# Performance work log

Hardware: AMD Instinct MI355X
Metric: run time of the kernel (lower is better)

The kernel has to match this reference:

```python
import jax, jax.numpy as jnp
import numpy as np

D_IN = 1024
D_OUT = 1024
NUM_HEADS = 16
HEAD_DIM = D_OUT // NUM_HEADS


def setup_inputs() -> dict:
    key = jax.random.key(0)
    ks = jax.random.split(key, 6)
    scale = 0.02
    x = jax.random.normal(ks[0], (2, 2048, D_IN), dtype=jnp.float32)
    Wq = jax.random.normal(ks[1], (D_IN, D_OUT), dtype=jnp.float32) * scale
    Wk = jax.random.normal(ks[2], (D_IN, D_OUT), dtype=jnp.float32) * scale
    Wv = jax.random.normal(ks[3], (D_IN, D_OUT), dtype=jnp.float32) * scale
    Wo = jax.random.normal(ks[4], (D_OUT, D_OUT), dtype=jnp.float32) * scale
    bo = jax.random.normal(ks[5], (D_OUT,), dtype=jnp.float32) * scale
    return {"x": x, "Wq": Wq, "Wk": Wk, "Wv": Wv, "Wo": Wo, "bo": bo}


def reference(x, Wq, Wk, Wv, Wo, bo):
    b, T, _ = x.shape
    h, dh = NUM_HEADS, HEAD_DIM
    # QKV projections (no bias), split heads: [b,T,d_out] -> [b,h,T,dh]
    q = (x @ Wq).reshape(b, T, h, dh).transpose(0, 2, 1, 3)
    k = (x @ Wk).reshape(b, T, h, dh).transpose(0, 2, 1, 3)
    v = (x @ Wv).reshape(b, T, h, dh).transpose(0, 2, 1, 3)
    # scaled dot-product scores with causal mask
    scores = jnp.einsum("bhqd,bhkd->bhqk", q, k) / jnp.sqrt(jnp.float32(dh))
    causal = jnp.tril(jnp.ones((T, T), dtype=bool))  # True = allowed
    scores = jnp.where(causal, scores, -jnp.inf)
    attn = jax.nn.softmax(scores, axis=-1)
    # dropout p=0.0 -> identity
    ctx = jnp.einsum("bhqk,bhkd->bhqd", attn, v)
    ctx = ctx.transpose(0, 2, 1, 3).reshape(b, T, h * dh)
    return ctx @ Wo + bo
```

## Files before the change

kernel.cpp:

```cpp
#include <hip/hip_runtime.h>

typedef __attribute__((ext_vector_type(8))) __bf16 bf16x8;
typedef __attribute__((ext_vector_type(4))) __bf16 bf16x4;
typedef __attribute__((ext_vector_type(4))) float  f32x4;

static constexpr int TSEQ    = 2048;
static constexpr int DMODEL  = 1024;
static constexpr int HD      = 64;
static constexpr int VSTRIDE = 2080;

#define AS1 __attribute__((address_space(1)))
#define AS3 __attribute__((address_space(3)))
#define SW(r) ((((r) & 12) >> 1) | ((r) & 1))

__global__ __launch_bounds__(256) void k_prep(const float* __restrict__ x,
    const float* __restrict__ w0, const float* __restrict__ w1,
    const float* __restrict__ w2, const float* __restrict__ w3,
    __bf16* __restrict__ xbf, __bf16* __restrict__ wt_all) {
  __shared__ float tile[32][33];
  const int blk = blockIdx.x;
  const int tid = threadIdx.x;
  if (blk < 4096) {
    size_t i = ((size_t)blk * 256 + tid) * 4;
    float4 v = *(const float4*)(x + i);
    bf16x4 o = { (__bf16)v.x, (__bf16)v.y, (__bf16)v.z, (__bf16)v.w };
    *(bf16x4*)(xbf + i) = o;
    return;
  }
  const int tz = blk - 4096;
  const int wi = tz >> 10;
  const int tl = tz & 1023;
  const int n0 = (tl & 31) * 32, k0 = (tl >> 5) * 32;
  const float* w = wi == 0 ? w0 : wi == 1 ? w1 : wi == 2 ? w2 : w3;
  __bf16* out = wt_all + (size_t)wi * DMODEL * DMODEL;
  const int tx = tid & 31, ty0 = (tid >> 5) * 4;
#pragma unroll
  for (int j = 0; j < 4; j++)
    tile[ty0 + j][tx] = w[(size_t)(k0 + ty0 + j) * DMODEL + n0 + tx];
  __syncthreads();
#pragma unroll
  for (int j = 0; j < 4; j++)
    out[(size_t)(n0 + ty0 + j) * DMODEL + k0 + tx] = (__bf16)tile[tx][ty0 + j];
}

__device__ __forceinline__ void gemm_mainloop(const __bf16* __restrict__ A,
                                              const __bf16* __restrict__ Bt,
                                              int bm, int bn,
                                              __bf16* At, __bf16* Bl,
                                              f32x4 acc[4][4]) {
  const int tid  = threadIdx.x;
  const int lane = tid & 63;
  const int l15  = lane & 15, quad = lane >> 4;
  const int wv   = tid >> 6;
  const int wm   = (wv >> 1) * 64, wn = (wv & 1) * 64;
  const int s0   = wv * 2;
  const int srow = lane >> 2;
  const int scol = (lane & 3) << 3;
  for (int k0 = 0; k0 < 1024; k0 += 32) {
    __syncthreads();
#pragma unroll
    for (int ss = 0; ss < 2; ss++) {
      const int s   = s0 + ss;
      const int row = s * 16 + srow;
      const __bf16* ga = A  + (size_t)(bm + row) * 1024 + k0 + scol;
      const __bf16* gb = Bt + (size_t)(bn + row) * 1024 + k0 + scol;
      __builtin_amdgcn_global_load_lds((const AS1 void*)ga,
                                       (AS3 void*)(At + s * 512), 16, 0, 0);
      __builtin_amdgcn_global_load_lds((const AS1 void*)gb,
                                       (AS3 void*)(Bl + s * 512), 16, 0, 0);
    }
    __syncthreads();
    bf16x8 af[4], bfr[4];
#pragma unroll
    for (int mt = 0; mt < 4; mt++)
      af[mt] = *(const bf16x8*)(At + (wm + mt * 16 + l15) * 32 + quad * 8);
#pragma unroll
    for (int nt = 0; nt < 4; nt++)
      bfr[nt] = *(const bf16x8*)(Bl + (wn + nt * 16 + l15) * 32 + quad * 8);
#pragma unroll
    for (int mt = 0; mt < 4; mt++)
#pragma unroll
      for (int nt = 0; nt < 4; nt++)
        acc[mt][nt] = __builtin_amdgcn_mfma_f32_16x16x32_bf16(
            af[mt], bfr[nt], acc[mt][nt], 0, 0, 0);
  }
}

__global__ __launch_bounds__(256) void k_gemm_qkv(const __bf16* __restrict__ xbf,
    const __bf16* __restrict__ wt_all, __bf16* __restrict__ qws,
    __bf16* __restrict__ kws, __bf16* __restrict__ vtws) {
  __shared__ __bf16 At[128 * 32];
  __shared__ __bf16 Bl[128 * 32];
  const int which = blockIdx.z;
  const __bf16* wt = wt_all + (size_t)which * DMODEL * DMODEL;
  const int bm = blockIdx.y * 128, bn = blockIdx.x * 128;
  f32x4 acc[4][4];
  const f32x4 z = {0.f, 0.f, 0.f, 0.f};
#pragma unroll
  for (int mt = 0; mt < 4; mt++)
#pragma unroll
    for (int nt = 0; nt < 4; nt++) acc[mt][nt] = z;
  gemm_mainloop(xbf, wt, bm, bn, At, Bl, acc);
  const int lane = threadIdx.x & 63;
  const int l15 = lane & 15, quad = lane >> 4;
  const int wv = threadIdx.x >> 6;
  const int wm = (wv >> 1) * 64, wn = (wv & 1) * 64;
#pragma unroll
  for (int mt = 0; mt < 4; mt++)
#pragma unroll
    for (int nt = 0; nt < 4; nt++)
#pragma unroll
      for (int r = 0; r < 4; r++) {
        int m = bm + wm + mt * 16 + quad * 4 + r;
        int n = bn + wn + nt * 16 + l15;
        int b = m >> 11, t = m & 2047;
        int h = n >> 6,  d = n & 63;
        int bh = b * 16 + h;
        float av = acc[mt][nt][r];
        if (which == 0)      qws[((size_t)bh * TSEQ + t) * HD + d] = (__bf16)(av * 0.18033688f);
        else if (which == 1) kws[((size_t)bh * TSEQ + t) * HD + d] = (__bf16)av;
        else                 vtws[((size_t)bh * HD + d) * VSTRIDE + t] = (__bf16)av;
      }
}

__global__ __launch_bounds__(256) void k_attn(const __bf16* __restrict__ qws,
    const __bf16* __restrict__ kws, const __bf16* __restrict__ vtws,
    __bf16* __restrict__ ctx) {
  const int bh = blockIdx.x & 31;
  const int a  = 15 - (blockIdx.x >> 5);
  const int tcnt = 2 * a + 2;
  const int tid = threadIdx.x;
  const int lane = tid & 63, wv = tid >> 6;
  const int l15 = lane & 15, quad = lane >> 4;
  const __bf16* qp = qws  + (size_t)bh * TSEQ * HD;
  const __bf16* kp = kws  + (size_t)bh * TSEQ * HD;
  const __bf16* vp = vtws + (size_t)bh * HD * VSTRIDE;
  const int b = bh >> 4, h = bh & 15;
  const int qbase = a * 128 + wv * 32;

  __shared__ __align__(16) __bf16 kbuf[2][64 * 64];
  __shared__ __align__(16) __bf16 vbuf[2][64 * 64];
  __shared__ __align__(16) __bf16 plds[4][32 * 64];

  const int sr = tid >> 3;
  const int c8 = tid & 7;

  bf16x8 aq[2][2];
#pragma unroll
  for (int mt = 0; mt < 2; mt++)
#pragma unroll
    for (int kb = 0; kb < 2; kb++)
      aq[mt][kb] = *(const bf16x8*)(qp + (size_t)(qbase + mt * 16 + l15) * HD + kb * 32 + quad * 8);

  bf16x8 kreg[2], vreg[2];
  kreg[0] = *(const bf16x8*)(kp + (size_t)sr * HD + c8 * 8);
  kreg[1] = *(const bf16x8*)(kp + (size_t)(sr + 32) * HD + c8 * 8);
  vreg[0] = *(const bf16x8*)(vp + (size_t)sr * VSTRIDE + c8 * 8);
  vreg[1] = *(const bf16x8*)(vp + (size_t)(sr + 32) * VSTRIDE + c8 * 8);
  *(bf16x8*)(kbuf[0] + sr * 64 + ((c8 ^ SW(sr)) << 3))             = kreg[0];
  *(bf16x8*)(kbuf[0] + (sr + 32) * 64 + ((c8 ^ SW(sr + 32)) << 3)) = kreg[1];
  *(bf16x8*)(vbuf[0] + sr * 64 + ((c8 ^ SW(sr)) << 3))             = vreg[0];
  *(bf16x8*)(vbuf[0] + (sr + 32) * 64 + ((c8 ^ SW(sr + 32)) << 3)) = vreg[1];
  __syncthreads();

  float lpart[2][4] = {{0.f, 0.f, 0.f, 0.f}, {0.f, 0.f, 0.f, 0.f}};
  const f32x4 z = {0.f, 0.f, 0.f, 0.f};
  f32x4 acc[2][4];
#pragma unroll
  for (int mt = 0; mt < 2; mt++)
#pragma unroll
    for (int dt = 0; dt < 4; dt++) acc[mt][dt] = z;

  for (int t = 0; t < tcnt; t++) {
    const int cur = t & 1;
    if (t + 1 < tcnt) {
      const int ktn = (t + 1) * 64;
      kreg[0] = *(const bf16x8*)(kp + (size_t)(ktn + sr) * HD + c8 * 8);
      kreg[1] = *(const bf16x8*)(kp + (size_t)(ktn + sr + 32) * HD + c8 * 8);
      vreg[0] = *(const bf16x8*)(vp + (size_t)sr * VSTRIDE + ktn + c8 * 8);
      vreg[1] = *(const bf16x8*)(vp + (size_t)(sr + 32) * VSTRIDE + ktn + c8 * 8);
    }

    const bool skipall = (t * 64) > (qbase + 31);
    if (!skipall) {
      const bool full = (t * 64 + 63) <= qbase;
      f32x4 sarr[2][4];
#pragma unroll
      for (int mt = 0; mt < 2; mt++)
#pragma unroll
        for (int nt = 0; nt < 4; nt++) sarr[mt][nt] = z;
#pragma unroll
      for (int kb = 0; kb < 2; kb++)
#pragma unroll
        for (int nt = 0; nt < 4; nt++) {
          const int row = nt * 16 + l15;
          bf16x8 bk = *(const bf16x8*)(kbuf[cur] + row * 64 + (((kb * 4 + quad) ^ SW(row)) << 3));
#pragma unroll
          for (int mt = 0; mt < 2; mt++)
            sarr[mt][nt] = __builtin_amdgcn_mfma_f32_16x16x32_bf16(aq[mt][kb], bk, sarr[mt][nt], 0, 0, 0);
        }
      if (full) {
#pragma unroll
        for (int mt = 0; mt < 2; mt++)
#pragma unroll
          for (int r = 0; r < 4; r++) {
            const int prow = mt * 16 + quad * 4 + r;
#pragma unroll
            for (int nt = 0; nt < 4; nt++) {
              float p = __builtin_amdgcn_exp2f(sarr[mt][nt][r]);
              lpart[mt][r] += p;
              plds[wv][prow * 64 + ((nt * 16 + l15) ^ (SW(prow) << 3))] = (__bf16)p;
            }
          }
      } else {
#pragma unroll
        for (int mt = 0; mt < 2; mt++)
#pragma unroll
          for (int r = 0; r < 4; r++) {
            const int prow = mt * 16 + quad * 4 + r;
            const int qglob = qbase + prow;
#pragma unroll
            for (int nt = 0; nt < 4; nt++) {
              const int kglob = t * 64 + nt * 16 + l15;
              float p = (kglob <= qglob) ? __builtin_amdgcn_exp2f(sarr[mt][nt][r]) : 0.f;
              lpart[mt][r] += p;
              plds[wv][prow * 64 + ((nt * 16 + l15) ^ (SW(prow) << 3))] = (__bf16)p;
            }
          }
      }
#pragma unroll
      for (int kb = 0; kb < 2; kb++) {
        bf16x8 pa[2];
#pragma unroll
        for (int mt = 0; mt < 2; mt++) {
          const int row = mt * 16 + l15;
          pa[mt] = *(const bf16x8*)(&plds[wv][row * 64 + (((kb * 4 + quad) ^ SW(row)) << 3)]);
        }
#pragma unroll
        for (int dt = 0; dt < 4; dt++) {
          const int rowv = dt * 16 + l15;
          bf16x8 bv = *(const bf16x8*)(vbuf[cur] + rowv * 64 + (((kb * 4 + quad) ^ SW(rowv)) << 3));
#pragma unroll
          for (int mt = 0; mt < 2; mt++)
            acc[mt][dt] = __builtin_amdgcn_mfma_f32_16x16x32_bf16(pa[mt], bv, acc[mt][dt], 0, 0, 0);
        }
      }
    }

    if (t + 1 < tcnt) {
      const int nxt = cur ^ 1;
      *(bf16x8*)(kbuf[nxt] + sr * 64 + ((c8 ^ SW(sr)) << 3))             = kreg[0];
      *(bf16x8*)(kbuf[nxt] + (sr + 32) * 64 + ((c8 ^ SW(sr + 32)) << 3)) = kreg[1];
      *(bf16x8*)(vbuf[nxt] + sr * 64 + ((c8 ^ SW(sr)) << 3))             = vreg[0];
      *(bf16x8*)(vbuf[nxt] + (sr + 32) * 64 + ((c8 ^ SW(sr + 32)) << 3)) = vreg[1];
    }
    __syncthreads();
  }

#pragma unroll
  for (int mt = 0; mt < 2; mt++)
#pragma unroll
    for (int r = 0; r < 4; r++) {
      float l = lpart[mt][r];
      l += __shfl_xor(l, 1, 64);
      l += __shfl_xor(l, 2, 64);
      l += __shfl_xor(l, 4, 64);
      l += __shfl_xor(l, 8, 64);
      const float linv = 1.f / l;
      const int qrow = qbase + mt * 16 + quad * 4 + r;
#pragma unroll
      for (int dt = 0; dt < 4; dt++)
        ctx[((size_t)(b * TSEQ + qrow)) * DMODEL + h * 64 + dt * 16 + l15] =
            (__bf16)(acc[mt][dt][r] * linv);
    }
}

__global__ __launch_bounds__(256) void k_gemm_out(const __bf16* __restrict__ ctx,
    const __bf16* __restrict__ wot, const float* __restrict__ bo,
    float* __restrict__ out) {
  __shared__ __bf16 At[128 * 32];
  __shared__ __bf16 Bl[128 * 32];
  const int bm = blockIdx.y * 128, bn = blockIdx.x * 128;
  f32x4 acc[4][4];
  const f32x4 z = {0.f, 0.f, 0.f, 0.f};
#pragma unroll
  for (int mt = 0; mt < 4; mt++)
#pragma unroll
    for (int nt = 0; nt < 4; nt++) acc[mt][nt] = z;
  gemm_mainloop(ctx, wot, bm, bn, At, Bl, acc);
  const int lane = threadIdx.x & 63;
  const int l15 = lane & 15, quad = lane >> 4;
  const int wv = threadIdx.x >> 6;
  const int wm = (wv >> 1) * 64, wn = (wv & 1) * 64;
#pragma unroll
  for (int mt = 0; mt < 4; mt++)
#pragma unroll
    for (int nt = 0; nt < 4; nt++)
#pragma unroll
      for (int r = 0; r < 4; r++) {
        int m = bm + wm + mt * 16 + quad * 4 + r;
        int n = bn + wn + nt * 16 + l15;
        out[(size_t)m * DMODEL + n] = acc[mt][nt][r] + bo[n];
      }
}

extern "C" void kernel_launch(void* const* d_in, const int* in_sizes, int n_in,
                              void* d_out, int out_size, void* d_ws, size_t ws_size,
                              hipStream_t stream) {
  const float* x  = (const float*)d_in[0];
  const float* Wq = (const float*)d_in[1];
  const float* Wk = (const float*)d_in[2];
  const float* Wv = (const float*)d_in[3];
  const float* Wo = (const float*)d_in[4];
  const float* bo = (const float*)d_in[5];
  float* out = (float*)d_out;

  __bf16* xbf  = (__bf16*)d_ws;
  __bf16* wt   = xbf  + (size_t)4096 * 1024;
  __bf16* qws  = wt   + (size_t)4 * 1024 * 1024;
  __bf16* kws  = qws  + (size_t)32 * 2048 * 64;
  __bf16* vtws = kws  + (size_t)32 * 2048 * 64;
  __bf16* ctx  = xbf;

  k_prep<<<8192, 256, 0, stream>>>(x, Wq, Wk, Wv, Wo, xbf, wt);
  k_gemm_qkv<<<dim3(8, 32, 3), 256, 0, stream>>>(xbf, wt, qws, kws, vtws);
  k_attn<<<512, 256, 0, stream>>>(qws, kws, vtws, ctx);
  k_gemm_out<<<dim3(8, 32), 256, 0, stream>>>(ctx, wt + (size_t)3 * 1024 * 1024, bo, out);
}
```

Baseline: 200.1 us.

## Switch attention to 32x32 MFMA with transposed scores, register-resident P

Rewrites the attention inner loop to use 32x32x16 bf16 MFMA and computes S^T (K as A operand, Q as B), so each lane holds one query column. The probabilities are packed to bf16 and exchanged across half-waves with shuffles instead of going through the per-wave LDS P buffer. It also changes block-to-tile ordering so heavy and light causal tiles interleave. This removes the LDS round trip and cuts MFMA instruction count, at the cost of cross-lane shuffles and inline asm for packing.

```diff
diff --git a/kernel.cpp b/kernel.cpp
--- a/kernel.cpp
+++ b/kernel.cpp
@@ -1,8 +1,10 @@
 #include <hip/hip_runtime.h>
 
-typedef __attribute__((ext_vector_type(8))) __bf16 bf16x8;
-typedef __attribute__((ext_vector_type(4))) __bf16 bf16x4;
-typedef __attribute__((ext_vector_type(4))) float  f32x4;
+typedef __attribute__((ext_vector_type(8)))  __bf16 bf16x8;
+typedef __attribute__((ext_vector_type(4)))  __bf16 bf16x4;
+typedef __attribute__((ext_vector_type(4)))  float  f32x4;
+typedef __attribute__((ext_vector_type(16))) float  f32x16;
+typedef __attribute__((ext_vector_type(4)))  int    i32x4;
 
 static constexpr int TSEQ    = 2048;
 static constexpr int DMODEL  = 1024;
@@ -127,30 +129,29 @@
     const __bf16* __restrict__ kws, const __bf16* __restrict__ vtws,
     __bf16* __restrict__ ctx) {
   const int bh = blockIdx.x & 31;
-  const int a  = 15 - (blockIdx.x >> 5);
+  const int tr = blockIdx.x >> 5;
+  const int a  = (tr < 8) ? (15 - tr) : (tr - 8);
   const int tcnt = 2 * a + 2;
   const int tid = threadIdx.x;
   const int lane = tid & 63, wv = tid >> 6;
-  const int l15 = lane & 15, quad = lane >> 4;
+  const int l31 = lane & 31, hi = lane >> 5;
   const __bf16* qp = qws  + (size_t)bh * TSEQ * HD;
   const __bf16* kp = kws  + (size_t)bh * TSEQ * HD;
   const __bf16* vp = vtws + (size_t)bh * HD * VSTRIDE;
   const int b = bh >> 4, h = bh & 15;
   const int qbase = a * 128 + wv * 32;
+  const int qg    = qbase + l31;
 
   __shared__ __align__(16) __bf16 kbuf[2][64 * 64];
   __shared__ __align__(16) __bf16 vbuf[2][64 * 64];
-  __shared__ __align__(16) __bf16 plds[4][32 * 64];
 
   const int sr = tid >> 3;
   const int c8 = tid & 7;
 
-  bf16x8 aq[2][2];
-#pragma unroll
-  for (int mt = 0; mt < 2; mt++)
-#pragma unroll
-    for (int kb = 0; kb < 2; kb++)
-      aq[mt][kb] = *(const bf16x8*)(qp + (size_t)(qbase + mt * 16 + l15) * HD + kb * 32 + quad * 8);
+  bf16x8 aq[4];
+#pragma unroll
+  for (int s = 0; s < 4; s++)
+    aq[s] = *(const bf16x8*)(qp + (size_t)qg * HD + s * 16 + hi * 8);
 
   bf16x8 kreg[2], vreg[2];
   kreg[0] = *(const bf16x8*)(kp + (size_t)sr * HD + c8 * 8);
@@ -163,13 +164,10 @@
   *(bf16x8*)(vbuf[0] + (sr + 32) * 64 + ((c8 ^ SW(sr + 32)) << 3)) = vreg[1];
   __syncthreads();
 
-  float lpart[2][4] = {{0.f, 0.f, 0.f, 0.f}, {0.f, 0.f, 0.f, 0.f}};
-  const f32x4 z = {0.f, 0.f, 0.f, 0.f};
-  f32x4 acc[2][4];
-#pragma unroll
-  for (int mt = 0; mt < 2; mt++)
-#pragma unroll
-    for (int dt = 0; dt < 4; dt++) acc[mt][dt] = z;
+  const f32x16 z16 = {0.f,0.f,0.f,0.f,0.f,0.f,0.f,0.f,0.f,0.f,0.f,0.f,0.f,0.f,0.f,0.f};
+  float lpart = 0.f;
+  f32x16 acc[2];
+  acc[0] = z16; acc[1] = z16;
 
   for (int t = 0; t < tcnt; t++) {
     const int cur = t & 1;
@@ -184,65 +182,55 @@
     const bool skipall = (t * 64) > (qbase + 31);
     if (!skipall) {
       const bool full = (t * 64 + 63) <= qbase;
-      f32x4 sarr[2][4];
-#pragma unroll
-      for (int mt = 0; mt < 2; mt++)
-#pragma unroll
-        for (int nt = 0; nt < 4; nt++) sarr[mt][nt] = z;
-#pragma unroll
-      for (int kb = 0; kb < 2; kb++)
-#pragma unroll
-        for (int nt = 0; nt < 4; nt++) {
-          const int row = nt * 16 + l15;
-          bf16x8 bk = *(const bf16x8*)(kbuf[cur] + row * 64 + (((kb * 4 + quad) ^ SW(row)) << 3));
-#pragma unroll
-          for (int mt = 0; mt < 2; mt++)
-            sarr[mt][nt] = __builtin_amdgcn_mfma_f32_16x16x32_bf16(aq[mt][kb], bk, sarr[mt][nt], 0, 0, 0);
+      const __bf16* kb_ = kbuf[cur];
+      const __bf16* vb_ = vbuf[cur];
+#pragma unroll
+      for (int kt = 0; kt < 2; kt++) {
+        f32x16 s = z16;
+#pragma unroll
+        for (int ds = 0; ds < 4; ds++) {
+          const int krow = kt * 32 + l31;
+          bf16x8 ak = *(const bf16x8*)(kb_ + krow * 64 + (((ds * 2 + hi) ^ SW(krow)) << 3));
+          s = __builtin_amdgcn_mfma_f32_32x32x16_bf16(ak, aq[ds], s, 0, 0, 0);
         }
-      if (full) {
-#pragma unroll
-        for (int mt = 0; mt < 2; mt++)
-#pragma unroll
-          for (int r = 0; r < 4; r++) {
-            const int prow = mt * 16 + quad * 4 + r;
-#pragma unroll
-            for (int nt = 0; nt < 4; nt++) {
-              float p = __builtin_amdgcn_exp2f(sarr[mt][nt][r]);
-              lpart[mt][r] += p;
-              plds[wv][prow * 64 + ((nt * 16 + l15) ^ (SW(prow) << 3))] = (__bf16)p;
-            }
+        float pv[16];
+        if (full) {
+#pragma unroll
+          for (int r = 0; r < 16; r++) {
+            pv[r] = __builtin_amdgcn_exp2f(s[r]);
+            lpart += pv[r];
           }
-      } else {
-#pragma unroll
-        for (int mt = 0; mt < 2; mt++)
-#pragma unroll
-          for (int r = 0; r < 4; r++) {
-            const int prow = mt * 16 + quad * 4 + r;
-            const int qglob = qbase + prow;
-#pragma unroll
-            for (int nt = 0; nt < 4; nt++) {
-              const int kglob = t * 64 + nt * 16 + l15;
-              float p = (kglob <= qglob) ? __builtin_amdgcn_exp2f(sarr[mt][nt][r]) : 0.f;
-              lpart[mt][r] += p;
-              plds[wv][prow * 64 + ((nt * 16 + l15) ^ (SW(prow) << 3))] = (__bf16)p;
-            }
+        } else {
+#pragma unroll
+          for (int r = 0; r < 16; r++) {
+            const int kg = t * 64 + kt * 32 + (r & 3) + 8 * (r >> 2) + 4 * hi;
+            float p = (kg <= qg) ? __builtin_amdgcn_exp2f(s[r]) : 0.f;
+            pv[r] = p;
+            lpart += p;
           }
-      }
-#pragma unroll
-      for (int kb = 0; kb < 2; kb++) {
-        bf16x8 pa[2];
-#pragma unroll
-        for (int mt = 0; mt < 2; mt++) {
-          const int row = mt * 16 + l15;
-          pa[mt] = *(const bf16x8*)(&plds[wv][row * 64 + (((kb * 4 + quad) ^ SW(row)) << 3)]);
         }
-#pragma unroll
-        for (int dt = 0; dt < 4; dt++) {
-          const int rowv = dt * 16 + l15;
-          bf16x8 bv = *(const bf16x8*)(vbuf[cur] + rowv * 64 + (((kb * 4 + quad) ^ SW(rowv)) << 3));
-#pragma unroll
-          for (int mt = 0; mt < 2; mt++)
-            acc[mt][dt] = __builtin_amdgcn_mfma_f32_16x16x32_bf16(pa[mt], bv, acc[mt][dt], 0, 0, 0);
+        int c[8];
+#pragma unroll
+        for (int j = 0; j < 8; j++) {
+          int w;
+          asm("v_cvt_pk_bf16_f32 %0, %1, %2" : "=v"(w) : "v"(pv[2 * j]), "v"(pv[2 * j + 1]));
+          c[j] = w;
+        }
+        const int oc0 = __shfl_xor(c[0], 32, 64), oc1 = __shfl_xor(c[1], 32, 64);
+        const int oc2 = __shfl_xor(c[2], 32, 64), oc3 = __shfl_xor(c[3], 32, 64);
+        const int oc4 = __shfl_xor(c[4], 32, 64), oc5 = __shfl_xor(c[5], 32, 64);
+        const int oc6 = __shfl_xor(c[6], 32, 64), oc7 = __shfl_xor(c[7], 32, 64);
+        i32x4 w0 = { hi ? oc2 : c[0], hi ? oc3 : c[1], hi ? c[2] : oc0, hi ? c[3] : oc1 };
+        i32x4 w1 = { hi ? oc6 : c[4], hi ? oc7 : c[5], hi ? c[6] : oc4, hi ? c[7] : oc5 };
+        bf16x8 pa0 = __builtin_bit_cast(bf16x8, w0);
+        bf16x8 pa1 = __builtin_bit_cast(bf16x8, w1);
+#pragma unroll
+        for (int dt = 0; dt < 2; dt++) {
+          const int vrow = dt * 32 + l31;
+          bf16x8 bv0 = *(const bf16x8*)(vb_ + vrow * 64 + (((kt * 4 + 0 + hi) ^ SW(vrow)) << 3));
+          acc[dt] = __builtin_amdgcn_mfma_f32_32x32x16_bf16(pa0, bv0, acc[dt], 0, 0, 0);
+          bf16x8 bv1 = *(const bf16x8*)(vb_ + vrow * 64 + (((kt * 4 + 2 + hi) ^ SW(vrow)) << 3));
+          acc[dt] = __builtin_amdgcn_mfma_f32_32x32x16_bf16(pa1, bv1, acc[dt], 0, 0, 0);
         }
       }
     }
@@ -257,22 +245,17 @@
     __syncthreads();
   }
 
-#pragma unroll
-  for (int mt = 0; mt < 2; mt++)
-#pragma unroll
-    for (int r = 0; r < 4; r++) {
-      float l = lpart[mt][r];
-      l += __shfl_xor(l, 1, 64);
-      l += __shfl_xor(l, 2, 64);
-      l += __shfl_xor(l, 4, 64);
-      l += __shfl_xor(l, 8, 64);
-      const float linv = 1.f / l;
-      const int qrow = qbase + mt * 16 + quad * 4 + r;
-#pragma unroll
-      for (int dt = 0; dt < 4; dt++)
-        ctx[((size_t)(b * TSEQ + qrow)) * DMODEL + h * 64 + dt * 16 + l15] =
-            (__bf16)(acc[mt][dt][r] * linv);
-    }
+  const float lfull = lpart + __shfl_xor(lpart, 32, 64);
+#pragma unroll
+  for (int r = 0; r < 16; r++) {
+    const int ql = (r & 3) + 8 * (r >> 2) + 4 * hi;
+    const float linv = 1.f / __shfl(lfull, ql, 64);
+    const int qrow = qbase + ql;
+#pragma unroll
+    for (int dt = 0; dt < 2; dt++)
+      ctx[((size_t)(b * TSEQ + qrow)) * DMODEL + h * 64 + dt * 32 + l31] =
+          (__bf16)(acc[dt][r] * linv);
+  }
 }
 
 __global__ __launch_bounds__(256) void k_gemm_out(const __bf16* __restrict__ ctx,
```

Measured after the change: 195.4 us. -2.4%, faster.
